# Kernel tuning notes

Hardware: AMD Instinct MI355X
Metric: run time of the kernel (lower is better)

## Reference

```python
import jax, jax.numpy as jnp
import numpy as np

EPS = 1e-5
NUM_HEADS = 12
MAX_TEXT_LEN = 40

def ln(x, g, b):
    m = x.mean(-1, keepdims=True)
    v = ((x - m) ** 2).mean(-1, keepdims=True)
    return (x - m) / jnp.sqrt(v + EPS) * g + b

def mlp(x, w1, b1, w2, b2):
    h = jax.nn.gelu(x @ w1.T + b1, approximate=False)  # torch nn.GELU default = exact
    return h @ w2.T + b2

def setup_inputs() -> dict:
    key = jax.random.key(0)
    ks = jax.random.split(key, 16)
    B, N, C, H, HID = 16, 616, 768, 12, 3072
    s = 0.02
    d = {}
    d["x"] = jax.random.normal(ks[0], (B, N, C), jnp.float32)
    d["rel_bias"] = jax.random.normal(ks[1], (H, N, N), jnp.float32)
    d["ln1_g"] = jnp.ones(C, jnp.float32); d["ln1_b"] = jnp.zeros(C, jnp.float32)
    d["w_qkv"] = jax.random.normal(ks[2], (3 * C, C), jnp.float32) * s
    d["q_bias"] = jnp.zeros(C, jnp.float32); d["v_bias"] = jnp.zeros(C, jnp.float32)
    d["w_proj"] = jax.random.normal(ks[3], (C, C), jnp.float32) * s
    d["b_proj"] = jnp.zeros(C, jnp.float32)
    d["gamma1"] = 0.1 * jnp.ones(C, jnp.float32)
    d["gamma2"] = 0.1 * jnp.ones(C, jnp.float32)
    d["ln2t_g"] = jnp.ones(C, jnp.float32); d["ln2t_b"] = jnp.zeros(C, jnp.float32)
    d["ln2i_g"] = jnp.ones(C, jnp.float32); d["ln2i_b"] = jnp.zeros(C, jnp.float32)
    d["wt1"] = jax.random.normal(ks[4], (HID, C), jnp.float32) * s
    d["bt1"] = jnp.zeros(HID, jnp.float32)
    d["wt2"] = jax.random.normal(ks[5], (C, HID), jnp.float32) * s
    d["bt2"] = jnp.zeros(C, jnp.float32)
    d["wi1"] = jax.random.normal(ks[6], (HID, C), jnp.float32) * s
    d["bi1"] = jnp.zeros(HID, jnp.float32)
    d["wi2"] = jax.random.normal(ks[7], (C, HID), jnp.float32) * s
    d["bi2"] = jnp.zeros(C, jnp.float32)
    return d

def reference(x, rel_bias, ln1_g, ln1_b, w_qkv, q_bias, v_bias, w_proj, b_proj,
              gamma1, gamma2, ln2t_g, ln2t_b, ln2i_g, ln2i_b,
              wt1, bt1, wt2, bt2, wi1, bi1, wi2, bi2):
    B, N, C = x.shape
    H = NUM_HEADS
    hd = C // H
    scale = hd ** -0.5
    # --- attention ---
    n = ln(x, ln1_g, ln1_b)
    qkv_bias = jnp.concatenate([q_bias, jnp.zeros_like(v_bias), v_bias])
    qkv = (n @ w_qkv.T + qkv_bias).reshape(B, N, 3, H, hd).transpose(2, 0, 3, 1, 4)
    q, k, v = qkv[0] * scale, qkv[1], qkv[2]  # [B,H,N,hd]
    attn = jnp.einsum('bhqd,bhkd->bhqk', q.astype(jnp.float32), k.astype(jnp.float32))
    attn = attn + rel_bias  # rel_bias [H,N,N] broadcasts over B
    attn = jax.nn.softmax(attn, axis=-1).astype(x.dtype)
    o = jnp.einsum('bhqk,bhkd->bhqd', attn, v).transpose(0, 2, 1, 3).reshape(B, N, C)
    o = o @ w_proj.T + b_proj
    x = x + gamma1 * o
    # --- modality-split MLP (modality_type is None, no vl-ffn) ---
    xt = x[:, :MAX_TEXT_LEN]
    xi = x[:, MAX_TEXT_LEN:]
    xt = xt + gamma2 * mlp(ln(xt, ln2t_g, ln2t_b), wt1, bt1, wt2, bt2)
    xi = xi + gamma2 * mlp(ln(xi, ln2i_g, ln2i_b), wi1, bi1, wi2, bi2)
    return jnp.concatenate([xt, xi], axis=1)
```

## Files before the change

kernel.cpp:

```cpp
#include <hip/hip_runtime.h>
#include <hip/hip_bf16.h>
#include <stdint.h>
#include <math.h>

#define AS1 __attribute__((address_space(1)))
#define AS3 __attribute__((address_space(3)))

typedef __bf16 bf16_t;
typedef __bf16 bf16x8 __attribute__((ext_vector_type(8)));
typedef float f32x4 __attribute__((ext_vector_type(4)));

static constexpr int B_ = 16, N_ = 616, C_ = 768, H_ = 12, HD = 64, HID = 3072;
static constexpr int NP = 640;
static constexpr int M_REAL = B_ * N_;
static constexpr int M_PAD = 9984;
static constexpr int NT_ = 40, NI_ = 576;

__device__ __forceinline__ void gl_lds16(const void* g, void* l) {
  __builtin_amdgcn_global_load_lds((const AS1 void*)(uintptr_t)g,
                                   (AS3 void*)(uint32_t)(uintptr_t)l, 16, 0, 0);
}
__device__ __forceinline__ f32x4 mfma16(bf16x8 a, bf16x8 b, f32x4 c) {
  return __builtin_amdgcn_mfma_f32_16x16x32_bf16(a, b, c, 0, 0, 0);
}
__device__ __forceinline__ float gelu_f(float x) {
  float u = x * (0.7978845608f + 0.0356774081f * x * x);
  return x / (1.f + __expf(-2.f * u));
}

struct CastArgs {
  const float* src[7];
  bf16_t* dst[7];
  int n4[7];
};

__global__ __launch_bounds__(256) void cast_all(CastArgs a, int total4) {
  int i = blockIdx.x * blockDim.x + threadIdx.x;
  int st = gridDim.x * blockDim.x;
  for (; i < total4; i += st) {
    int off = i;
#pragma unroll
    for (int s = 0; s < 7; ++s) {
      if (off < a.n4[s]) {
        float4 v = ((const float4*)a.src[s])[off];
        float sub = (s == 6) ? 8.f : 0.f;
        bf16_t* d = a.dst[s] + (size_t)off * 4;
        d[0] = (bf16_t)(v.x - sub); d[1] = (bf16_t)(v.y - sub);
        d[2] = (bf16_t)(v.z - sub); d[3] = (bf16_t)(v.w - sub);
        break;
      }
      off -= a.n4[s];
    }
  }
}

__global__ __launch_bounds__(256) void ln_rows(const float* __restrict__ x,
                                               const float* __restrict__ g,
                                               const float* __restrict__ b,
                                               bf16_t* __restrict__ out) {
  int r = blockIdx.x, t = threadIdx.x;
  bf16_t* orow = out + (size_t)r * C_;
  const float* xr = x + (size_t)r * C_;
  float v0 = xr[t], v1 = xr[t + 256], v2 = xr[t + 512];
  float s = v0 + v1 + v2, ss = v0 * v0 + v1 * v1 + v2 * v2;
#pragma unroll
  for (int off = 32; off > 0; off >>= 1) { s += __shfl_xor(s, off); ss += __shfl_xor(ss, off); }
  __shared__ float sm[8];
  int w = t >> 6;
  if ((t & 63) == 0) { sm[w] = s; sm[4 + w] = ss; }
  __syncthreads();
  s = sm[0] + sm[1] + sm[2] + sm[3];
  ss = sm[4] + sm[5] + sm[6] + sm[7];
  float mean = s * (1.f / C_);
  float var = ss * (1.f / C_) - mean * mean;
  float ri = rsqrtf(var + 1e-5f);
  orow[t]       = (bf16_t)((v0 - mean) * ri * g[t]       + b[t]);
  orow[t + 256] = (bf16_t)((v1 - mean) * ri * g[t + 256] + b[t + 256]);
  orow[t + 512] = (bf16_t)((v2 - mean) * ri * g[t + 512] + b[t + 512]);
}

__global__ __launch_bounds__(256) void ln2_pack(const float* __restrict__ x1,
                                                const float* __restrict__ gt, const float* __restrict__ bt,
                                                const float* __restrict__ gi, const float* __restrict__ bi,
                                                bf16_t* __restrict__ out) {
  int m = blockIdx.x, t = threadIdx.x;
  if (m >= M_REAL) {
    bf16_t* orow = out + (size_t)(640 + (m - M_REAL)) * C_;
    orow[t] = (bf16_t)0.f; orow[t+256] = (bf16_t)0.f; orow[t+512] = (bf16_t)0.f;
    return;
  }
  int b_ = m / N_, nn = m - b_ * N_;
  const float* g; const float* bb; int dest;
  if (nn < NT_) { dest = b_ * NT_ + nn; g = gt; bb = bt; }
  else          { dest = 768 + b_ * NI_ + (nn - NT_); g = gi; bb = bi; }
  const float* xr = x1 + (size_t)m * C_;
  float v0 = xr[t], v1 = xr[t + 256], v2 = xr[t + 512];
  float s = v0 + v1 + v2, ss = v0 * v0 + v1 * v1 + v2 * v2;
#pragma unroll
  for (int off = 32; off > 0; off >>= 1) { s += __shfl_xor(s, off); ss += __shfl_xor(ss, off); }
  __shared__ float sm[8];
  int w = t >> 6;
  if ((t & 63) == 0) { sm[w] = s; sm[4 + w] = ss; }
  __syncthreads();
  s = sm[0] + sm[1] + sm[2] + sm[3];
  ss = sm[4] + sm[5] + sm[6] + sm[7];
  float mean = s * (1.f / C_);
  float var = ss * (1.f / C_) - mean * mean;
  float ri = rsqrtf(var + 1e-5f);
  bf16_t* orow = out + (size_t)dest * C_;
  orow[t]       = (bf16_t)((v0 - mean) * ri * g[t]       + bb[t]);
  orow[t + 256] = (bf16_t)((v1 - mean) * ri * g[t + 256] + bb[t + 256]);
  orow[t + 512] = (bf16_t)((v2 - mean) * ri * g[t + 512] + bb[t + 512]);
}

__global__ __launch_bounds__(256) void transpose_v(const bf16_t* __restrict__ v,
                                                   bf16_t* __restrict__ vT) {
  __shared__ bf16_t t[64][80];
  int n0 = blockIdx.x * 64, bh = blockIdx.y;
  int tid = threadIdx.x;
  int r0 = tid >> 2, c0 = (tid & 3) * 16;
  int n = n0 + r0;
#pragma unroll
  for (int cc = 0; cc < 2; ++cc) {
    bf16x8 vv;
    if (n < N_) vv = *(const bf16x8*)(v + ((size_t)bh * N_ + n) * HD + c0 + cc * 8);
    else {
#pragma unroll
      for (int e = 0; e < 8; ++e) vv[e] = (bf16_t)0.f;
    }
#pragma unroll
    for (int e = 0; e < 8; ++e) t[c0 + cc * 8 + e][r0] = vv[e];
  }
  __syncthreads();
  int d = tid >> 2, nc = (tid & 3) * 16;
  bf16_t* dst = vT + ((size_t)(bh * HD + d)) * NP + n0 + nc;
  *(bf16x8*)dst       = *(const bf16x8*)&t[d][nc];
  *(bf16x8*)(dst + 8) = *(const bf16x8*)&t[d][nc + 8];
}

struct EpiP {
  const float* bias;
  const float* bias_i;
  const float* bias2;
  const float* gamma;
  const float* xres;
  float* outf;
  bf16_t* ob0;
  bf16_t* ob1;
  bf16_t* ob2;
};

template <int EPI>
__global__ __launch_bounds__(256, 4) void gemm64(const bf16_t* __restrict__ A,
                                                 const bf16_t* __restrict__ Bt,
                                                 const bf16_t* __restrict__ Bi,
                                                 int K, int MBc, int nb, int tb, EpiP P) {
  __shared__ bf16_t As[4096], Bs[8192];
  const int tid = threadIdx.x, lane = tid & 63, w = tid >> 6;
  const int l16 = lane & 15, lq = lane >> 4;
  const int NTk = K >> 6;

  int mblk, nblk;
  {
    int nwg = MBc * nb;
    int bid = blockIdx.x;
    int q8 = nwg >> 3, r8 = nwg & 7;
    int xcd = bid & 7, sidx = bid >> 3;
    int wg = (xcd < r8 ? xcd * (q8 + 1) : r8 * (q8 + 1) + (xcd - r8) * q8) + sidx;
    mblk = wg / nb; nblk = wg - mblk * nb;
  }
  const int m0 = mblk * 64, n0 = nblk * 128;
  const bf16_t* Bw = (mblk < tb) ? Bt : Bi;

  f32x4 acc[4][2] = {};

  const int swsrc = ((lane & 7) ^ ((lane >> 3) & 7)) * 8;
  size_t aoff[2]; int aldso[2];
  size_t boff[4]; int bldso[4];
#pragma unroll
  for (int j = 0; j < 2; ++j) {
    int srow = w * 16 + j * 8 + (lane >> 3);
    aoff[j] = (size_t)(m0 + srow) * K + swsrc;
    aldso[j] = (w * 128 + j * 64) * 8;
  }
#pragma unroll
  for (int j = 0; j < 4; ++j) {
    int srow = w * 32 + j * 8 + (lane >> 3);
    boff[j] = (size_t)(n0 + srow) * K + swsrc;
    bldso[j] = (w * 256 + j * 64) * 8;
  }
  const int sw0 = ((0 * 4 + lq) ^ (l16 & 7)) * 8;
  const int sw1 = ((1 * 4 + lq) ^ (l16 & 7)) * 8;
  const int rbA = l16 * 64;
  const int rbB = (w * 32 + l16) * 64;

  for (int t = 0; t < NTk; ++t) {
    const size_t kadd = (size_t)t * 64;
#pragma unroll
    for (int j = 0; j < 2; ++j) gl_lds16(A + aoff[j] + kadd, As + aldso[j]);
#pragma unroll
    for (int j = 0; j < 4; ++j) gl_lds16(Bw + boff[j] + kadd, Bs + bldso[j]);
    __syncthreads();

    bf16x8 av[4][2], bv[2][2];
#pragma unroll
    for (int i = 0; i < 4; ++i) {
      av[i][0] = *(const bf16x8*)(As + rbA + i * 1024 + sw0);
      av[i][1] = *(const bf16x8*)(As + rbA + i * 1024 + sw1);
    }
#pragma unroll
    for (int j = 0; j < 2; ++j) {
      bv[j][0] = *(const bf16x8*)(Bs + rbB + j * 1024 + sw0);
      bv[j][1] = *(const bf16x8*)(Bs + rbB + j * 1024 + sw1);
    }
#pragma unroll
    for (int kk = 0; kk < 2; ++kk)
#pragma unroll
      for (int i = 0; i < 4; ++i)
#pragma unroll
        for (int j = 0; j < 2; ++j)
          acc[i][j] = mfma16(av[i][kk], bv[j][kk], acc[i][j]);
    __syncthreads();
  }

  const float* bsel = (mblk < tb) ? P.bias : P.bias_i;
  (void)bsel;
  int which = n0 / C_;
#pragma unroll
  for (int i = 0; i < 4; ++i) {
    int mb = m0 + i * 16 + lq * 4;
#pragma unroll
    for (int j = 0; j < 2; ++j) {
      int jc = n0 + w * 32 + j * 16 + l16;
#pragma unroll
      for (int rr = 0; rr < 4; ++rr) {
        int m = mb + rr;
        float v = acc[i][j][rr];
        if constexpr (EPI == 0) {
          int b_ = m / N_, nn = m - b_ * N_;
          int jj = jc - which * C_;
          int hh = jj >> 6, d = jj & 63;
          int bh = b_ * H_ + hh;
          if (which == 0) {
            P.ob0[((size_t)bh * NP + nn) * HD + d] = (bf16_t)((v + P.bias[jj]) * 0.125f);
          } else if (which == 1) {
            P.ob1[((size_t)bh * NP + nn) * HD + d] = (bf16_t)v;
          } else {
            P.ob2[((size_t)bh * N_ + nn) * HD + d] = (bf16_t)(v + P.bias2[jj]);
          }
        } else if constexpr (EPI == 1) {
          size_t idx = (size_t)m * C_ + jc;
          P.outf[idx] = P.xres[idx] + P.gamma[jc] * (v + P.bias[jc]);
        } else if constexpr (EPI == 2) {
          P.ob0[(size_t)m * HID + jc] = (bf16_t)gelu_f(v + bsel[jc]);
        } else {
          int orig = -1;
          if (m < 640)      orig = (m / NT_) * N_ + (m - (m / NT_) * NT_);
          else if (m >= 768) {
            int mi = m - 768;
            int bb = mi / NI_;
            orig = bb * N_ + NT_ + (mi - bb * NI_);
          }
          if (orig >= 0) {
            size_t idx = (size_t)orig * C_ + jc;
            P.outf[idx] = P.xres[idx] + P.gamma[jc] * (v + bsel[jc]);
          }
        }
      }
    }
  }
}

__global__ __launch_bounds__(256) void attn_fwd(const bf16_t* __restrict__ qb,
                                                const bf16_t* __restrict__ kb,
                                                const bf16_t* __restrict__ vT,
                                                const bf16_t* __restrict__ biasb,
                                                bf16_t* __restrict__ o_mat) {
  __shared__ bf16_t qs[64 * 64];
  __shared__ bf16_t ks[2][64 * 64], vs[2][64 * 64];
  __shared__ bf16_t ps[4][16 * 72];
  const int tid = threadIdx.x, lane = tid & 63, w = tid >> 6;
  const int l16 = lane & 15, lq = lane >> 4;
  int wg = (blockIdx.x & 7) * 240 + (blockIdx.x >> 3);
  const int qt = wg % 10;
  const int rb = wg / 10;
  const int b_ = rb & 15, h = rb >> 4;
  const int bh = b_ * H_ + h;
  const int q0 = qt * 64;
  const int swr = (l16 & 7);
  constexpr int NKT = NP / 64;

  const bf16_t* ksrc = kb + (size_t)bh * NP * HD;
  const bf16_t* vsrc = vT + (size_t)bh * HD * NP;

  auto stage_kv = [&](int c, int kt) {
    int n0k = kt * 64;
#pragma unroll
    for (int it = 0; it < 2; ++it) {
      int cb = it * 256 + w * 64, cc = cb + lane;
      int row = cc >> 3, sg = (cc & 7) ^ ((cc >> 3) & 7);
      gl_lds16(ksrc + ((size_t)(n0k + row)) * HD + sg * 8, ks[c] + cb * 8);
      gl_lds16(vsrc + (size_t)row * NP + n0k + sg * 8, vs[c] + cb * 8);
    }
  };

  const bf16_t* qsrc = qb + ((size_t)bh * NP + q0) * HD;
#pragma unroll
  for (int it = 0; it < 2; ++it) {
    int cb = it * 256 + w * 64, c = cb + lane;
    int row = c >> 3, sg = (c & 7) ^ ((c >> 3) & 7);
    gl_lds16(qsrc + row * 64 + sg * 8, qs + cb * 8);
  }
  stage_kv(0, 0);
  __syncthreads();

  bf16x8 aq[2];
  aq[0] = *(const bf16x8*)(qs + (w * 16 + l16) * 64 + ((0 * 4 + lq) ^ swr) * 8);
  aq[1] = *(const bf16x8*)(qs + (w * 16 + l16) * 64 + ((1 * 4 + lq) ^ swr) * 8);

  float lsum[4] = {0.f, 0.f, 0.f, 0.f};
  f32x4 oacc[4] = {};
  const int qrow_base = q0 + w * 16 + lq * 4;

  const bf16_t* bp[4];
#pragma unroll
  for (int r = 0; r < 4; ++r) {
    int qg = qrow_base + r;
    int qc = qg < N_ ? qg : (N_ - 1);
    bp[r] = biasb + (size_t)h * N_ * N_ + (size_t)qc * N_;
  }

  for (int kt = 0; kt < NKT; ++kt) {
    const int c = kt & 1;
    if (kt > 0) __syncthreads();
    if (kt + 1 < NKT) stage_kv(c ^ 1, kt + 1);

    f32x4 sf[4];
#pragma unroll
    for (int f = 0; f < 4; ++f) {
      f32x4 z = {};
#pragma unroll
      for (int kk = 0; kk < 2; ++kk) {
        bf16x8 bk = *(const bf16x8*)(ks[c] + (f * 16 + l16) * 64 + ((kk * 4 + lq) ^ swr) * 8);
        z = mfma16(aq[kk], bk, z);
      }
      sf[f] = z;
    }

    int n0k = kt * 64;
    bf16_t* psw = ps[w];
    if (kt < NKT - 1) {
#pragma unroll
      for (int f = 0; f < 4; ++f) {
        int kc = n0k + f * 16 + l16;
#pragma unroll
        for (int r = 0; r < 4; ++r) {
          float p = __expf(sf[f][r] + (float)bp[r][kc]);
          lsum[r] += p;
          psw[(lq * 4 + r) * 72 + f * 16 + l16] = (bf16_t)p;
        }
      }
    } else {
#pragma unroll
      for (int f = 0; f < 4; ++f) {
        int kc = n0k + f * 16 + l16;
        bool ok = kc < N_;
        int kcs = ok ? kc : 0;
#pragma unroll
        for (int r = 0; r < 4; ++r) {
          float p = ok ? __expf(sf[f][r] + (float)bp[r][kcs]) : 0.f;
          lsum[r] += p;
          psw[(lq * 4 + r) * 72 + f * 16 + l16] = (bf16_t)p;
        }
      }
    }

#pragma unroll
    for (int kk = 0; kk < 2; ++kk) {
      bf16x8 pa = *(const bf16x8*)(psw + l16 * 72 + kk * 32 + lq * 8);
#pragma unroll
      for (int df = 0; df < 4; ++df) {
        bf16x8 bv = *(const bf16x8*)(vs[c] + (df * 16 + l16) * 64 + ((kk * 4 + lq) ^ swr) * 8);
        oacc[df] = mfma16(pa, bv, oacc[df]);
      }
    }
  }

#pragma unroll
  for (int off = 1; off < 16; off <<= 1)
#pragma unroll
    for (int r = 0; r < 4; ++r)
      lsum[r] += __shfl_xor(lsum[r], off, 16);

#pragma unroll
  for (int r = 0; r < 4; ++r) {
    int qg = qrow_base + r;
    if (qg < N_) {
      float rl = 1.f / lsum[r];
      size_t orow = ((size_t)(b_ * N_ + qg)) * C_ + h * HD;
#pragma unroll
      for (int df = 0; df < 4; ++df)
        o_mat[orow + df * 16 + l16] = (bf16_t)(oacc[df][r] * rl);
    }
  }
}

extern "C" void kernel_launch(void* const* d_in, const int* in_sizes, int n_in,
                              void* d_out, int out_size, void* d_ws, size_t ws_size,
                              hipStream_t stream) {
  const float* x      = (const float*)d_in[0];
  const float* rel    = (const float*)d_in[1];
  const float* ln1_g  = (const float*)d_in[2];
  const float* ln1_b  = (const float*)d_in[3];
  const float* w_qkv  = (const float*)d_in[4];
  const float* q_bias = (const float*)d_in[5];
  const float* v_bias = (const float*)d_in[6];
  const float* w_proj = (const float*)d_in[7];
  const float* b_proj = (const float*)d_in[8];
  const float* gamma1 = (const float*)d_in[9];
  const float* gamma2 = (const float*)d_in[10];
  const float* ln2t_g = (const float*)d_in[11];
  const float* ln2t_b = (const float*)d_in[12];
  const float* ln2i_g = (const float*)d_in[13];
  const float* ln2i_b = (const float*)d_in[14];
  const float* wt1    = (const float*)d_in[15];
  const float* bt1    = (const float*)d_in[16];
  const float* wt2    = (const float*)d_in[17];
  const float* bt2    = (const float*)d_in[18];
  const float* wi1    = (const float*)d_in[19];
  const float* bi1    = (const float*)d_in[20];
  const float* wi2    = (const float*)d_in[21];
  const float* bi2    = (const float*)d_in[22];
  float* out = (float*)d_out;

  char* ws = (char*)d_ws;
  bf16_t* wqkvb  = (bf16_t*)(ws + 0);
  bf16_t* wprojb = (bf16_t*)(ws + 3538944);
  bf16_t* wt1b   = (bf16_t*)(ws + 4718592);
  bf16_t* wi1b   = (bf16_t*)(ws + 9437184);
  bf16_t* wt2b   = (bf16_t*)(ws + 14155776);
  bf16_t* wi2b   = (bf16_t*)(ws + 18874368);
  bf16_t* n1     = (bf16_t*)(ws + 23592960);
  float*  x1     = (float*) (ws + 38928384);
  bf16_t* qbuf   = (bf16_t*)(ws + 69206016);
  bf16_t* kbuf   = (bf16_t*)(ws + 84934656);
  bf16_t* vTbuf  = (bf16_t*)(ws + 100663296);
  bf16_t* biasb  = (bf16_t*)(ws + 116391936);
  bf16_t* vtmp   = (bf16_t*)(ws + 38928384);
  bf16_t* o_mat  = n1;
  bf16_t* n2p    = n1;
  bf16_t* hbuf   = qbuf;

  {
    CastArgs a;
    a.src[0] = w_qkv;  a.dst[0] = wqkvb;  a.n4[0] = (3 * C_ * C_) / 4;
    a.src[1] = w_proj; a.dst[1] = wprojb; a.n4[1] = (C_ * C_) / 4;
    a.src[2] = wt1;    a.dst[2] = wt1b;   a.n4[2] = (HID * C_) / 4;
    a.src[3] = wi1;    a.dst[3] = wi1b;   a.n4[3] = (HID * C_) / 4;
    a.src[4] = wt2;    a.dst[4] = wt2b;   a.n4[4] = (C_ * HID) / 4;
    a.src[5] = wi2;    a.dst[5] = wi2b;   a.n4[5] = (C_ * HID) / 4;
    a.src[6] = rel;    a.dst[6] = biasb;  a.n4[6] = (H_ * N_ * N_) / 4;
    int total4 = a.n4[0] + a.n4[1] + a.n4[2] + a.n4[3] + a.n4[4] + a.n4[5] + a.n4[6];
    cast_all<<<2048, 256, 0, stream>>>(a, total4);
  }
  ln_rows<<<M_REAL, 256, 0, stream>>>(x, ln1_g, ln1_b, n1);

  {
    EpiP P{}; P.bias = q_bias; P.bias2 = v_bias;
    P.ob0 = qbuf; P.ob1 = kbuf; P.ob2 = vtmp;
    gemm64<0><<<154 * 18, 256, 0, stream>>>(n1, wqkvb, wqkvb, C_, 154, 18, 0, P);
  }
  transpose_v<<<dim3(NP / 64, B_ * H_), 256, 0, stream>>>(vtmp, vTbuf);
  attn_fwd<<<1920, 256, 0, stream>>>(qbuf, kbuf, vTbuf, biasb, o_mat);

  {
    EpiP P{}; P.bias = b_proj; P.bias_i = b_proj; P.gamma = gamma1; P.xres = x; P.outf = x1;
    gemm64<1><<<154 * 6, 256, 0, stream>>>(o_mat, wprojb, wprojb, C_, 154, 6, 0, P);
  }
  ln2_pack<<<M_PAD, 256, 0, stream>>>(x1, ln2t_g, ln2t_b, ln2i_g, ln2i_b, n2p);

  {
    EpiP P{}; P.bias = bt1; P.bias_i = bi1; P.ob0 = hbuf;
    gemm64<2><<<156 * 24, 256, 0, stream>>>(n2p, wt1b, wi1b, C_, 156, 24, 12, P);
  }
  {
    EpiP P{}; P.bias = bt2; P.bias_i = bi2; P.gamma = gamma2; P.xres = x1; P.outf = out;
    gemm64<3><<<156 * 6, 256, 0, stream>>>(hbuf, wt2b, wi2b, HID, 156, 6, 12, P);
  }
}
```

Before: 312.4 us.

## Widen GEMM N-tile to 192 and store mid-block residual in bf16

Enlarges the GEMM output tile from 64x128 to 64x192 so each wave computes three 16-wide column groups, raising data reuse per loaded A tile and cutting block count. Separately, the post-attention residual x1 is written and read as bf16 instead of fp32, halving its memory traffic in the projection epilogue, LayerNorm2 and final residual add. The bf16 residual reduces the precision of the skip connection that feeds the output, and the larger tile increases LDS and register use per block.

```diff
diff --git a/kernel.cpp b/kernel.cpp
--- a/kernel.cpp
+++ b/kernel.cpp
@@ -79,7 +79,7 @@
   orow[t + 512] = (bf16_t)((v2 - mean) * ri * g[t + 512] + b[t + 512]);
 }
 
-__global__ __launch_bounds__(256) void ln2_pack(const float* __restrict__ x1,
+__global__ __launch_bounds__(256) void ln2_pack(const bf16_t* __restrict__ x1,
                                                 const float* __restrict__ gt, const float* __restrict__ bt,
                                                 const float* __restrict__ gi, const float* __restrict__ bi,
                                                 bf16_t* __restrict__ out) {
@@ -93,8 +93,8 @@
   const float* g; const float* bb; int dest;
   if (nn < NT_) { dest = b_ * NT_ + nn; g = gt; bb = bt; }
   else          { dest = 768 + b_ * NI_ + (nn - NT_); g = gi; bb = bi; }
-  const float* xr = x1 + (size_t)m * C_;
-  float v0 = xr[t], v1 = xr[t + 256], v2 = xr[t + 512];
+  const bf16_t* xr = x1 + (size_t)m * C_;
+  float v0 = (float)xr[t], v1 = (float)xr[t + 256], v2 = (float)xr[t + 512];
   float s = v0 + v1 + v2, ss = v0 * v0 + v1 * v1 + v2 * v2;
 #pragma unroll
   for (int off = 32; off > 0; off >>= 1) { s += __shfl_xor(s, off); ss += __shfl_xor(ss, off); }
@@ -144,18 +144,20 @@
   const float* bias2;
   const float* gamma;
   const float* xres;
+  const bf16_t* xresb;
   float* outf;
+  bf16_t* outfb;
   bf16_t* ob0;
   bf16_t* ob1;
   bf16_t* ob2;
 };
 
 template <int EPI>
-__global__ __launch_bounds__(256, 4) void gemm64(const bf16_t* __restrict__ A,
-                                                 const bf16_t* __restrict__ Bt,
-                                                 const bf16_t* __restrict__ Bi,
-                                                 int K, int MBc, int nb, int tb, EpiP P) {
-  __shared__ bf16_t As[4096], Bs[8192];
+__global__ __launch_bounds__(256, 4) void gemm192(const bf16_t* __restrict__ A,
+                                                  const bf16_t* __restrict__ Bt,
+                                                  const bf16_t* __restrict__ Bi,
+                                                  int K, int MBc, int nb, int tb, EpiP P) {
+  __shared__ bf16_t As[4096], Bs[12288];
   const int tid = threadIdx.x, lane = tid & 63, w = tid >> 6;
   const int l16 = lane & 15, lq = lane >> 4;
   const int NTk = K >> 6;
@@ -169,14 +171,14 @@
     int wg = (xcd < r8 ? xcd * (q8 + 1) : r8 * (q8 + 1) + (xcd - r8) * q8) + sidx;
     mblk = wg / nb; nblk = wg - mblk * nb;
   }
-  const int m0 = mblk * 64, n0 = nblk * 128;
+  const int m0 = mblk * 64, n0 = nblk * 192;
   const bf16_t* Bw = (mblk < tb) ? Bt : Bi;
 
-  f32x4 acc[4][2] = {};
+  f32x4 acc[4][3] = {};
 
   const int swsrc = ((lane & 7) ^ ((lane >> 3) & 7)) * 8;
   size_t aoff[2]; int aldso[2];
-  size_t boff[4]; int bldso[4];
+  size_t boff[6]; int bldso[6];
 #pragma unroll
   for (int j = 0; j < 2; ++j) {
     int srow = w * 16 + j * 8 + (lane >> 3);
@@ -184,32 +186,32 @@
     aldso[j] = (w * 128 + j * 64) * 8;
   }
 #pragma unroll
-  for (int j = 0; j < 4; ++j) {
-    int srow = w * 32 + j * 8 + (lane >> 3);
+  for (int j = 0; j < 6; ++j) {
+    int srow = w * 48 + j * 8 + (lane >> 3);
     boff[j] = (size_t)(n0 + srow) * K + swsrc;
-    bldso[j] = (w * 256 + j * 64) * 8;
+    bldso[j] = (w * 384 + j * 64) * 8;
   }
   const int sw0 = ((0 * 4 + lq) ^ (l16 & 7)) * 8;
   const int sw1 = ((1 * 4 + lq) ^ (l16 & 7)) * 8;
   const int rbA = l16 * 64;
-  const int rbB = (w * 32 + l16) * 64;
+  const int rbB = (w * 48 + l16) * 64;
 
   for (int t = 0; t < NTk; ++t) {
     const size_t kadd = (size_t)t * 64;
 #pragma unroll
     for (int j = 0; j < 2; ++j) gl_lds16(A + aoff[j] + kadd, As + aldso[j]);
 #pragma unroll
-    for (int j = 0; j < 4; ++j) gl_lds16(Bw + boff[j] + kadd, Bs + bldso[j]);
+    for (int j = 0; j < 6; ++j) gl_lds16(Bw + boff[j] + kadd, Bs + bldso[j]);
     __syncthreads();
 
-    bf16x8 av[4][2], bv[2][2];
+    bf16x8 av[4][2], bv[3][2];
 #pragma unroll
     for (int i = 0; i < 4; ++i) {
       av[i][0] = *(const bf16x8*)(As + rbA + i * 1024 + sw0);
       av[i][1] = *(const bf16x8*)(As + rbA + i * 1024 + sw1);
     }
 #pragma unroll
-    for (int j = 0; j < 2; ++j) {
+    for (int j = 0; j < 3; ++j) {
       bv[j][0] = *(const bf16x8*)(Bs + rbB + j * 1024 + sw0);
       bv[j][1] = *(const bf16x8*)(Bs + rbB + j * 1024 + sw1);
     }
@@ -218,7 +220,7 @@
 #pragma unroll
       for (int i = 0; i < 4; ++i)
 #pragma unroll
-        for (int j = 0; j < 2; ++j)
+        for (int j = 0; j < 3; ++j)
           acc[i][j] = mfma16(av[i][kk], bv[j][kk], acc[i][j]);
     __syncthreads();
   }
@@ -230,8 +232,8 @@
   for (int i = 0; i < 4; ++i) {
     int mb = m0 + i * 16 + lq * 4;
 #pragma unroll
-    for (int j = 0; j < 2; ++j) {
-      int jc = n0 + w * 32 + j * 16 + l16;
+    for (int j = 0; j < 3; ++j) {
+      int jc = n0 + w * 48 + j * 16 + l16;
 #pragma unroll
       for (int rr = 0; rr < 4; ++rr) {
         int m = mb + rr;
@@ -250,7 +252,7 @@
           }
         } else if constexpr (EPI == 1) {
           size_t idx = (size_t)m * C_ + jc;
-          P.outf[idx] = P.xres[idx] + P.gamma[jc] * (v + P.bias[jc]);
+          P.outfb[idx] = (bf16_t)(P.xres[idx] + P.gamma[jc] * (v + P.bias[jc]));
         } else if constexpr (EPI == 2) {
           P.ob0[(size_t)m * HID + jc] = (bf16_t)gelu_f(v + bsel[jc]);
         } else {
@@ -263,7 +265,7 @@
           }
           if (orig >= 0) {
             size_t idx = (size_t)orig * C_ + jc;
-            P.outf[idx] = P.xres[idx] + P.gamma[jc] * (v + bsel[jc]);
+            P.outf[idx] = (float)P.xresb[idx] + P.gamma[jc] * (v + bsel[jc]);
           }
         }
       }
@@ -441,7 +443,7 @@
   bf16_t* wt2b   = (bf16_t*)(ws + 14155776);
   bf16_t* wi2b   = (bf16_t*)(ws + 18874368);
   bf16_t* n1     = (bf16_t*)(ws + 23592960);
-  float*  x1     = (float*) (ws + 38928384);
+  bf16_t* x1b    = (bf16_t*)(ws + 38928384);
   bf16_t* qbuf   = (bf16_t*)(ws + 69206016);
   bf16_t* kbuf   = (bf16_t*)(ws + 84934656);
   bf16_t* vTbuf  = (bf16_t*)(ws + 100663296);
@@ -468,23 +470,23 @@
   {
     EpiP P{}; P.bias = q_bias; P.bias2 = v_bias;
     P.ob0 = qbuf; P.ob1 = kbuf; P.ob2 = vtmp;
-    gemm64<0><<<154 * 18, 256, 0, stream>>>(n1, wqkvb, wqkvb, C_, 154, 18, 0, P);
+    gemm192<0><<<154 * 12, 256, 0, stream>>>(n1, wqkvb, wqkvb, C_, 154, 12, 0, P);
   }
   transpose_v<<<dim3(NP / 64, B_ * H_), 256, 0, stream>>>(vtmp, vTbuf);
   attn_fwd<<<1920, 256, 0, stream>>>(qbuf, kbuf, vTbuf, biasb, o_mat);
 
   {
-    EpiP P{}; P.bias = b_proj; P.bias_i = b_proj; P.gamma = gamma1; P.xres = x; P.outf = x1;
-    gemm64<1><<<154 * 6, 256, 0, stream>>>(o_mat, wprojb, wprojb, C_, 154, 6, 0, P);
-  }
-  ln2_pack<<<M_PAD, 256, 0, stream>>>(x1, ln2t_g, ln2t_b, ln2i_g, ln2i_b, n2p);
+    EpiP P{}; P.bias = b_proj; P.bias_i = b_proj; P.gamma = gamma1; P.xres = x; P.outfb = x1b;
+    gemm192<1><<<154 * 4, 256, 0, stream>>>(o_mat, wprojb, wprojb, C_, 154, 4, 0, P);
+  }
+  ln2_pack<<<M_PAD, 256, 0, stream>>>(x1b, ln2t_g, ln2t_b, ln2i_g, ln2i_b, n2p);
 
   {
     EpiP P{}; P.bias = bt1; P.bias_i = bi1; P.ob0 = hbuf;
-    gemm64<2><<<156 * 24, 256, 0, stream>>>(n2p, wt1b, wi1b, C_, 156, 24, 12, P);
-  }
-  {
-    EpiP P{}; P.bias = bt2; P.bias_i = bi2; P.gamma = gamma2; P.xres = x1; P.outf = out;
-    gemm64<3><<<156 * 6, 256, 0, stream>>>(hbuf, wt2b, wi2b, HID, 156, 6, 12, P);
-  }
-}
+    gemm192<2><<<156 * 16, 256, 0, stream>>>(n2p, wt1b, wi1b, C_, 156, 16, 12, P);
+  }
+  {
+    EpiP P{}; P.bias = bt2; P.bias_i = bi2; P.gamma = gamma2; P.xresb = x1b; P.outf = out;
+    gemm192<3><<<156 * 4, 256, 0, stream>>>(hbuf, wt2b, wi2b, HID, 156, 4, 12, P);
+  }
+}
```

New measurement: 306.1 us. 1.02x faster.

## Double-buffer GEMM LDS tiles and store residual x1 in bf16

Applied to the files above, without the earlier changes.

The GEMM main loop now uses two LDS buffers, issuing the global-to-LDS load for the next K tile before computing on the current one. This drops one barrier per iteration and overlaps memory with MFMA work. The occupancy hint falls from 4 to 3 blocks per CU because of the doubled shared memory. Separately, the post-attention residual x1 is written and read as bf16 instead of fp32, halving its traffic through ln2_pack and the final epilogue at the cost of residual-stream precision.

```diff
diff --git a/kernel.cpp b/kernel.cpp
--- a/kernel.cpp
+++ b/kernel.cpp
@@ -79,7 +79,7 @@
   orow[t + 512] = (bf16_t)((v2 - mean) * ri * g[t + 512] + b[t + 512]);
 }
 
-__global__ __launch_bounds__(256) void ln2_pack(const float* __restrict__ x1,
+__global__ __launch_bounds__(256) void ln2_pack(const bf16_t* __restrict__ x1,
                                                 const float* __restrict__ gt, const float* __restrict__ bt,
                                                 const float* __restrict__ gi, const float* __restrict__ bi,
                                                 bf16_t* __restrict__ out) {
@@ -93,8 +93,8 @@
   const float* g; const float* bb; int dest;
   if (nn < NT_) { dest = b_ * NT_ + nn; g = gt; bb = bt; }
   else          { dest = 768 + b_ * NI_ + (nn - NT_); g = gi; bb = bi; }
-  const float* xr = x1 + (size_t)m * C_;
-  float v0 = xr[t], v1 = xr[t + 256], v2 = xr[t + 512];
+  const bf16_t* xr = x1 + (size_t)m * C_;
+  float v0 = (float)xr[t], v1 = (float)xr[t + 256], v2 = (float)xr[t + 512];
   float s = v0 + v1 + v2, ss = v0 * v0 + v1 * v1 + v2 * v2;
 #pragma unroll
   for (int off = 32; off > 0; off >>= 1) { s += __shfl_xor(s, off); ss += __shfl_xor(ss, off); }
@@ -144,18 +144,20 @@
   const float* bias2;
   const float* gamma;
   const float* xres;
+  const bf16_t* xresb;
   float* outf;
+  bf16_t* outfb;
   bf16_t* ob0;
   bf16_t* ob1;
   bf16_t* ob2;
 };
 
 template <int EPI>
-__global__ __launch_bounds__(256, 4) void gemm64(const bf16_t* __restrict__ A,
+__global__ __launch_bounds__(256, 3) void gemm64(const bf16_t* __restrict__ A,
                                                  const bf16_t* __restrict__ Bt,
                                                  const bf16_t* __restrict__ Bi,
                                                  int K, int MBc, int nb, int tb, EpiP P) {
-  __shared__ bf16_t As[4096], Bs[8192];
+  __shared__ bf16_t As[2][4096], Bs[2][8192];
   const int tid = threadIdx.x, lane = tid & 63, w = tid >> 6;
   const int l16 = lane & 15, lq = lane >> 4;
   const int NTk = K >> 6;
@@ -194,24 +196,33 @@
   const int rbA = l16 * 64;
   const int rbB = (w * 32 + l16) * 64;
 
+  auto STAGE = [&](int c, int t) {
+    const size_t kadd = (size_t)t * 64;
+#pragma unroll
+    for (int j = 0; j < 2; ++j) gl_lds16(A + aoff[j] + kadd, &As[c][0] + aldso[j]);
+#pragma unroll
+    for (int j = 0; j < 4; ++j) gl_lds16(Bw + boff[j] + kadd, &Bs[c][0] + bldso[j]);
+  };
+
+  STAGE(0, 0);
+  __syncthreads();
+
   for (int t = 0; t < NTk; ++t) {
-    const size_t kadd = (size_t)t * 64;
-#pragma unroll
-    for (int j = 0; j < 2; ++j) gl_lds16(A + aoff[j] + kadd, As + aldso[j]);
-#pragma unroll
-    for (int j = 0; j < 4; ++j) gl_lds16(Bw + boff[j] + kadd, Bs + bldso[j]);
-    __syncthreads();
-
+    const int c = t & 1;
+    if (t + 1 < NTk) STAGE(c ^ 1, t + 1);
+
+    const bf16_t* Ac = &As[c][0];
+    const bf16_t* Bc = &Bs[c][0];
     bf16x8 av[4][2], bv[2][2];
 #pragma unroll
     for (int i = 0; i < 4; ++i) {
-      av[i][0] = *(const bf16x8*)(As + rbA + i * 1024 + sw0);
-      av[i][1] = *(const bf16x8*)(As + rbA + i * 1024 + sw1);
+      av[i][0] = *(const bf16x8*)(Ac + rbA + i * 1024 + sw0);
+      av[i][1] = *(const bf16x8*)(Ac + rbA + i * 1024 + sw1);
     }
 #pragma unroll
     for (int j = 0; j < 2; ++j) {
-      bv[j][0] = *(const bf16x8*)(Bs + rbB + j * 1024 + sw0);
-      bv[j][1] = *(const bf16x8*)(Bs + rbB + j * 1024 + sw1);
+      bv[j][0] = *(const bf16x8*)(Bc + rbB + j * 1024 + sw0);
+      bv[j][1] = *(const bf16x8*)(Bc + rbB + j * 1024 + sw1);
     }
 #pragma unroll
     for (int kk = 0; kk < 2; ++kk)
@@ -220,7 +231,8 @@
 #pragma unroll
         for (int j = 0; j < 2; ++j)
           acc[i][j] = mfma16(av[i][kk], bv[j][kk], acc[i][j]);
-    __syncthreads();
+
+    if (t + 1 < NTk) __syncthreads();
   }
 
   const float* bsel = (mblk < tb) ? P.bias : P.bias_i;
@@ -250,7 +262,7 @@
           }
         } else if constexpr (EPI == 1) {
           size_t idx = (size_t)m * C_ + jc;
-          P.outf[idx] = P.xres[idx] + P.gamma[jc] * (v + P.bias[jc]);
+          P.outfb[idx] = (bf16_t)(P.xres[idx] + P.gamma[jc] * (v + P.bias[jc]));
         } else if constexpr (EPI == 2) {
           P.ob0[(size_t)m * HID + jc] = (bf16_t)gelu_f(v + bsel[jc]);
         } else {
@@ -263,7 +275,7 @@
           }
           if (orig >= 0) {
             size_t idx = (size_t)orig * C_ + jc;
-            P.outf[idx] = P.xres[idx] + P.gamma[jc] * (v + bsel[jc]);
+            P.outf[idx] = (float)P.xresb[idx] + P.gamma[jc] * (v + bsel[jc]);
           }
         }
       }
@@ -441,7 +453,7 @@
   bf16_t* wt2b   = (bf16_t*)(ws + 14155776);
   bf16_t* wi2b   = (bf16_t*)(ws + 18874368);
   bf16_t* n1     = (bf16_t*)(ws + 23592960);
-  float*  x1     = (float*) (ws + 38928384);
+  bf16_t* x1b    = (bf16_t*)(ws + 38928384);
   bf16_t* qbuf   = (bf16_t*)(ws + 69206016);
   bf16_t* kbuf   = (bf16_t*)(ws + 84934656);
   bf16_t* vTbuf  = (bf16_t*)(ws + 100663296);
@@ -474,17 +486,17 @@
   attn_fwd<<<1920, 256, 0, stream>>>(qbuf, kbuf, vTbuf, biasb, o_mat);
 
   {
-    EpiP P{}; P.bias = b_proj; P.bias_i = b_proj; P.gamma = gamma1; P.xres = x; P.outf = x1;
+    EpiP P{}; P.bias = b_proj; P.bias_i = b_proj; P.gamma = gamma1; P.xres = x; P.outfb = x1b;
     gemm64<1><<<154 * 6, 256, 0, stream>>>(o_mat, wprojb, wprojb, C_, 154, 6, 0, P);
   }
-  ln2_pack<<<M_PAD, 256, 0, stream>>>(x1, ln2t_g, ln2t_b, ln2i_g, ln2i_b, n2p);
+  ln2_pack<<<M_PAD, 256, 0, stream>>>(x1b, ln2t_g, ln2t_b, ln2i_g, ln2i_b, n2p);
 
   {
     EpiP P{}; P.bias = bt1; P.bias_i = bi1; P.ob0 = hbuf;
     gemm64<2><<<156 * 24, 256, 0, stream>>>(n2p, wt1b, wi1b, C_, 156, 24, 12, P);
   }
   {
-    EpiP P{}; P.bias = bt2; P.bias_i = bi2; P.gamma = gamma2; P.xres = x1; P.outf = out;
+    EpiP P{}; P.bias = bt2; P.bias_i = bi2; P.gamma = gamma2; P.xresb = x1b; P.outf = out;
     gemm64<3><<<156 * 6, 256, 0, stream>>>(hbuf, wt2b, wi2b, HID, 156, 6, 12, P);
   }
 }
```

New measurement: 331.9 us. 6.2% more time.
